# Optimization experiments

Hardware: AMD Instinct MI355X
Metric: run time of the kernel (lower is better)

The kernel has to match this reference:

```python
import jax, jax.numpy as jnp
import numpy as np

B, K, D = 32768, 4096, 256


def setup_inputs() -> dict:
    key = jax.random.key(0)
    k1, k2 = jax.random.split(key)
    z_e_x = jax.random.normal(k1, (B, D), dtype=jnp.float32)
    # embedding.weight initialized N(0, 1) per init='normal'
    weight = jax.random.normal(k2, (K, D), dtype=jnp.float32)
    return {"z_e_x": z_e_x, "weight": weight}


def reference(z_e_x, weight):
    # Squared L2 distances ||z - e||^2 = ||z||^2 - 2 z.e + ||e||^2,
    # computed via a GEMM instead of materializing the [B, K, D] broadcast
    # that the torch code builds with repeat(). Same math as
    # sum((z_e_x_ - codebook_vectors)**2, dim=-1).
    z_sq = jnp.sum(z_e_x * z_e_x, axis=-1, keepdims=True)          # [B, 1]
    e_sq = jnp.sum(weight * weight, axis=-1)                        # [K]
    cross = jnp.einsum('bd,kd->bk', z_e_x, weight)                  # [B, K]
    distances = z_sq - 2.0 * cross + e_sq                           # [B, K]
    # greedy=True path of forward()
    index = jnp.argmin(distances, axis=-1)                          # [B] int
    # straight_through(): quantized lookup + straight-through estimator
    z_q_x = weight[index]                                           # [B, D]
    sg_z_e_x = z_e_x + jax.lax.stop_gradient(z_q_x - z_e_x)         # [B, D]
    return (sg_z_e_x, z_q_x, index)
```

## Files before the change

kernel.cpp:

```cpp
#include <hip/hip_runtime.h>

typedef _Float16 half8 __attribute__((ext_vector_type(8)));
typedef _Float16 half4 __attribute__((ext_vector_type(4)));
typedef float floatx16 __attribute__((ext_vector_type(16)));

constexpr int Bn = 32768, Kn = 4096, Dn = 256;
constexpr int BM = 128;
constexpr int BNS = 64;
constexpr int NI = Kn / BNS;
constexpr int NCH = NI * 4;
constexpr size_t W16_PLANE = (size_t)Kn * Dn * 2;

__global__ void prep_kernel(const float* __restrict__ w, float* __restrict__ esq,
                            _Float16* __restrict__ w16) {
    int code = blockIdx.x * 4 + (threadIdx.x >> 6);
    int lane = threadIdx.x & 63;
    float4 v = *reinterpret_cast<const float4*>(w + (size_t)code * Dn + lane * 4);
    float s = v.x * v.x + v.y * v.y + v.z * v.z + v.w * v.w;
    #pragma unroll
    for (int off = 32; off; off >>= 1) s += __shfl_xor(s, off);
    if (lane == 0) esq[code] = s;
    float fv[4] = {v.x, v.y, v.z, v.w};
    half4 h, l;
    #pragma unroll
    for (int j = 0; j < 4; ++j) {
        _Float16 hh = (_Float16)fv[j];
        h[j] = hh;
        l[j] = (_Float16)(fv[j] - (float)hh);
    }
    _Float16* hi = w16 + (size_t)code * Dn + lane * 4;
    *reinterpret_cast<half4*>(hi) = h;
    *reinterpret_cast<half4*>(hi + (size_t)Kn * Dn) = l;
}

#define GLDS(gsrc, ldsoff)                                                        \
    __builtin_amdgcn_global_load_lds(                                             \
        (const __attribute__((address_space(1))) unsigned int*)(const void*)(gsrc),\
        (__attribute__((address_space(3))) unsigned int*)(void*)(smem + (ldsoff)), \
        16, 0, 0)

__launch_bounds__(512, 2)
__global__ void vq_kernel(const float* __restrict__ z, const float* __restrict__ w,
                          const float* __restrict__ esq, const _Float16* __restrict__ w16,
                          float* __restrict__ out0, float* __restrict__ out1,
                          float* __restrict__ out2) {
    __shared__ char smem[84480];
    const int tid = threadIdx.x;
    const int wv_ = tid >> 6, l = tid & 63;
    const int mw = wv_ >> 1, nw = wv_ & 1;
    const int lh = l >> 5, ll = l & 31;
    const int blkRow = blockIdx.x * BM;

    float* esq_s = reinterpret_cast<float*>(smem + 65536);
    #pragma unroll
    for (int j = 0; j < 8; ++j) esq_s[j * 512 + tid] = esq[j * 512 + tid];

    half8 a_hi[16], a_lo[16];
    {
        const float* zr = z + (size_t)(blkRow + mw * 32 + ll) * Dn + lh * 8;
        #pragma unroll
        for (int ks = 0; ks < 16; ++ks) {
            float4 f0 = *reinterpret_cast<const float4*>(zr + ks * 16);
            float4 f1 = *reinterpret_cast<const float4*>(zr + ks * 16 + 4);
            float fv[8] = {f0.x, f0.y, f0.z, f0.w, f1.x, f1.y, f1.z, f1.w};
            #pragma unroll
            for (int j = 0; j < 8; ++j) {
                _Float16 h = (_Float16)fv[j];
                a_hi[ks][j] = h;
                a_lo[ks][j] = (_Float16)(fv[j] - (float)h);
            }
        }
    }

    const int sc = tid >> 3;
    const int se = ((tid & 7) * 16) ^ ((sc & 7) << 4);
    const char* srcH = reinterpret_cast<const char*>(w16) + (size_t)sc * 512 + se;
    const char* srcL = srcH + W16_PLANE;

    int vks[4];
    {
        const int c_loc = nw * 32 + ll;
        const int swz = (c_loc & 7) << 4;
        #pragma unroll
        for (int ks = 0; ks < 4; ++ks) vks[ks] = c_loc * 128 + ((ks * 32 + lh * 16) ^ swz);
    }

    float rbv[16];
    int rbi[16];
    #pragma unroll
    for (int q = 0; q < 16; ++q) { rbv[q] = 3.4e38f; rbi[q] = 0; }

    __syncthreads();

    GLDS(srcH, 0 + wv_ * 1024);
    GLDS(srcL, 0 + 8192 + wv_ * 1024);
    GLDS(srcH + 128, 16384 + wv_ * 1024);
    GLDS(srcL + 128, 16384 + 8192 + wv_ * 1024);

    for (int ni = 0; ni < NI; ++ni) {
        floatx16 acc = {};
        #pragma unroll
        for (int kc = 0; kc < 4; ++kc) {
            if (ni == NI - 1 && kc == 3) asm volatile("s_waitcnt vmcnt(0)" ::: "memory");
            else                         asm volatile("s_waitcnt vmcnt(2)" ::: "memory");
            __builtin_amdgcn_s_barrier();
            asm volatile("" ::: "memory");
            {
                const int c2 = ni * 4 + kc + 2;
                if (c2 < NCH) {
                    const size_t off2 = (size_t)(c2 >> 2) * 32768 + (size_t)(c2 & 3) * 128;
                    const int b2 = ((kc + 2) & 3) * 16384;
                    GLDS(srcH + off2, b2 + wv_ * 1024);
                    GLDS(srcL + off2, b2 + 8192 + wv_ * 1024);
                }
            }
            __builtin_amdgcn_s_setprio(1);
            #pragma unroll
            for (int ks = 0; ks < 4; ++ks) {
                const half8 bh = *reinterpret_cast<const half8*>(smem + kc * 16384 + vks[ks]);
                const half8 bl = *reinterpret_cast<const half8*>(smem + kc * 16384 + 8192 + vks[ks]);
                const half8 ah = a_hi[kc * 4 + ks];
                const half8 al = a_lo[kc * 4 + ks];
                acc = __builtin_amdgcn_mfma_f32_32x32x16_f16(ah, bh, acc, 0, 0, 0);
                acc = __builtin_amdgcn_mfma_f32_32x32x16_f16(ah, bl, acc, 0, 0, 0);
                acc = __builtin_amdgcn_mfma_f32_32x32x16_f16(al, bh, acc, 0, 0, 0);
            }
            __builtin_amdgcn_s_setprio(0);
        }
        const int col = ni * 64 + nw * 32 + ll;
        const float e = esq_s[col];
        #pragma unroll
        for (int q = 0; q < 16; ++q) {
            float v = fmaf(-2.f, acc[q], e);
            if (v < rbv[q]) { rbv[q] = v; rbi[q] = col; }
        }
    }

    #pragma unroll
    for (int off = 1; off < 32; off <<= 1) {
        #pragma unroll
        for (int q = 0; q < 16; ++q) {
            float ov = __shfl_xor(rbv[q], off);
            int oi = __shfl_xor(rbi[q], off);
            if (ov < rbv[q] || (ov == rbv[q] && oi < rbi[q])) { rbv[q] = ov; rbi[q] = oi; }
        }
    }

    int2* comb = reinterpret_cast<int2*>(smem + 81920);
    if (ll == 0) {
        #pragma unroll
        for (int q = 0; q < 16; ++q) {
            int row = mw * 32 + (q & 3) + 8 * (q >> 2) + 4 * lh;
            comb[row * 2 + nw] = make_int2(__float_as_int(rbv[q]), rbi[q]);
        }
    }
    __syncthreads();
    int* idxF = reinterpret_cast<int*>(smem + 83968);
    if (tid < 128) {
        int2 c0 = comb[tid * 2], c1 = comb[tid * 2 + 1];
        float v0 = __int_as_float(c0.x), v1 = __int_as_float(c1.x);
        idxF[tid] = (v1 < v0 || (v1 == v0 && c1.y < c0.y)) ? c1.y : c0.y;
    }
    __syncthreads();

    {
        const int r = tid >> 2, p4 = tid & 3;
        const int gRow = blkRow + r;
        const int idx = idxF[r];
        const float* wr = w + (size_t)idx * Dn + p4 * 64;
        const float* zr = z + (size_t)gRow * Dn + p4 * 64;
        float* o0 = out0 + (size_t)gRow * Dn + p4 * 64;
        float* o1 = out1 + (size_t)gRow * Dn + p4 * 64;
        #pragma unroll
        for (int q = 0; q < 16; ++q) {
            float4 wq = *reinterpret_cast<const float4*>(wr + q * 4);
            float4 zq = *reinterpret_cast<const float4*>(zr + q * 4);
            *reinterpret_cast<float4*>(o1 + q * 4) = wq;
            float4 sg;
            sg.x = zq.x + (wq.x - zq.x);
            sg.y = zq.y + (wq.y - zq.y);
            sg.z = zq.z + (wq.z - zq.z);
            sg.w = zq.w + (wq.w - zq.w);
            *reinterpret_cast<float4*>(o0 + q * 4) = sg;
        }
        if (p4 == 0) out2[gRow] = (float)idx;
    }
}

extern "C" void kernel_launch(void* const* d_in, const int* in_sizes, int n_in,
                              void* d_out, int out_size, void* d_ws, size_t ws_size,
                              hipStream_t stream) {
    (void)in_sizes; (void)n_in; (void)out_size; (void)ws_size;
    const float* z = (const float*)d_in[0];
    const float* w = (const float*)d_in[1];
    float* esq = (float*)d_ws;
    _Float16* w16 = (_Float16*)((char*)d_ws + 16384);
    float* out0 = (float*)d_out;
    float* out1 = out0 + (size_t)Bn * Dn;
    float* out2 = out1 + (size_t)Bn * Dn;

    prep_kernel<<<Kn / 4, 256, 0, stream>>>(w, esq, w16);
    vq_kernel<<<Bn / BM, 512, 0, stream>>>(z, w, esq, w16, out0, out1, out2);
}
```

Baseline: 291.3 us.

## Give each wave two 32-row M tiles and interleave hi/lo codebook planes

Halves the block to 4 waves, each computing two 32-row tiles so every LDS-loaded B fragment feeds twice as many MFMAs. Prep now writes the codebook hi/lo fp16 halves interleaved per row with a 16-way XOR swizzle, which changes the global-to-LDS load pattern and waits. The aim is fewer LDS reads per MFMA, at the cost of doubled A-fragment and argmin registers, lower occupancy (launch bounds 256,1), and fewer waves to hide latency.

```diff
diff --git a/kernel.cpp b/kernel.cpp
--- a/kernel.cpp
+++ b/kernel.cpp
@@ -9,28 +9,31 @@
 constexpr int BNS = 64;
 constexpr int NI = Kn / BNS;
 constexpr int NCH = NI * 4;
-constexpr size_t W16_PLANE = (size_t)Kn * Dn * 2;
 
 __global__ void prep_kernel(const float* __restrict__ w, float* __restrict__ esq,
-                            _Float16* __restrict__ w16) {
+                            char* __restrict__ w16) {
     int code = blockIdx.x * 4 + (threadIdx.x >> 6);
-    int lane = threadIdx.x & 63;
-    float4 v = *reinterpret_cast<const float4*>(w + (size_t)code * Dn + lane * 4);
+    int l = threadIdx.x & 63;
+    float4 v = *reinterpret_cast<const float4*>(w + (size_t)code * Dn + l * 4);
     float s = v.x * v.x + v.y * v.y + v.z * v.z + v.w * v.w;
     #pragma unroll
     for (int off = 32; off; off >>= 1) s += __shfl_xor(s, off);
-    if (lane == 0) esq[code] = s;
+    if (l == 0) esq[code] = s;
+
     float fv[4] = {v.x, v.y, v.z, v.w};
-    half4 h, l;
+    half4 h, lo;
     #pragma unroll
     for (int j = 0; j < 4; ++j) {
         _Float16 hh = (_Float16)fv[j];
         h[j] = hh;
-        l[j] = (_Float16)(fv[j] - (float)hh);
-    }
-    _Float16* hi = w16 + (size_t)code * Dn + lane * 4;
-    *reinterpret_cast<half4*>(hi) = h;
-    *reinterpret_cast<half4*>(hi + (size_t)Kn * Dn) = l;
+        lo[j] = (_Float16)(fv[j] - (float)hh);
+    }
+    const int kc = l >> 4;
+    const int o_h = (l & 15) * 8;
+    const int swz = (code & 15) << 4;
+    char* row = w16 + (size_t)code * 1024 + kc * 256;
+    *reinterpret_cast<half4*>(row + (o_h ^ swz)) = h;
+    *reinterpret_cast<half4*>(row + ((o_h + 128) ^ swz)) = lo;
 }
 
 #define GLDS(gsrc, ldsoff)                                                        \
@@ -39,25 +42,28 @@
         (__attribute__((address_space(3))) unsigned int*)(void*)(smem + (ldsoff)), \
         16, 0, 0)
 
-__launch_bounds__(512, 2)
+#define MFMA(a, b, c) __builtin_amdgcn_mfma_f32_32x32x16_f16((a), (b), (c), 0, 0, 0)
+
+__launch_bounds__(256, 1)
 __global__ void vq_kernel(const float* __restrict__ z, const float* __restrict__ w,
-                          const float* __restrict__ esq, const _Float16* __restrict__ w16,
+                          const float* __restrict__ esq, const char* __restrict__ w16,
                           float* __restrict__ out0, float* __restrict__ out1,
                           float* __restrict__ out2) {
     __shared__ char smem[84480];
     const int tid = threadIdx.x;
-    const int wv_ = tid >> 6, l = tid & 63;
-    const int mw = wv_ >> 1, nw = wv_ & 1;
+    const int wv = tid >> 6, l = tid & 63;
+    const int mw = wv >> 1, nw = wv & 1;
     const int lh = l >> 5, ll = l & 31;
     const int blkRow = blockIdx.x * BM;
 
     float* esq_s = reinterpret_cast<float*>(smem + 65536);
     #pragma unroll
-    for (int j = 0; j < 8; ++j) esq_s[j * 512 + tid] = esq[j * 512 + tid];
-
-    half8 a_hi[16], a_lo[16];
-    {
-        const float* zr = z + (size_t)(blkRow + mw * 32 + ll) * Dn + lh * 8;
+    for (int j = 0; j < 16; ++j) esq_s[j * 256 + tid] = esq[j * 256 + tid];
+
+    half8 a_hi[2][16], a_lo[2][16];
+    #pragma unroll
+    for (int t = 0; t < 2; ++t) {
+        const float* zr = z + (size_t)(blkRow + mw * 64 + t * 32 + ll) * Dn + lh * 8;
         #pragma unroll
         for (int ks = 0; ks < 16; ++ks) {
             float4 f0 = *reinterpret_cast<const float4*>(zr + ks * 16);
@@ -66,73 +72,85 @@
             #pragma unroll
             for (int j = 0; j < 8; ++j) {
                 _Float16 h = (_Float16)fv[j];
-                a_hi[ks][j] = h;
-                a_lo[ks][j] = (_Float16)(fv[j] - (float)h);
+                a_hi[t][ks][j] = h;
+                a_lo[t][ks][j] = (_Float16)(fv[j] - (float)h);
             }
         }
     }
 
-    const int sc = tid >> 3;
-    const int se = ((tid & 7) * 16) ^ ((sc & 7) << 4);
-    const char* srcH = reinterpret_cast<const char*>(w16) + (size_t)sc * 512 + se;
-    const char* srcL = srcH + W16_PLANE;
-
-    int vks[4];
+    const int G0 = wv * 256 + l;
+    const size_t srcOff0 = (size_t)(G0 >> 4) * 1024 + (G0 & 15) * 16;
+
+    int addrH[4], addrL[4];
     {
         const int c_loc = nw * 32 + ll;
-        const int swz = (c_loc & 7) << 4;
-        #pragma unroll
-        for (int ks = 0; ks < 4; ++ks) vks[ks] = c_loc * 128 + ((ks * 32 + lh * 16) ^ swz);
-    }
-
-    float rbv[16];
-    int rbi[16];
-    #pragma unroll
-    for (int q = 0; q < 16; ++q) { rbv[q] = 3.4e38f; rbi[q] = 0; }
-
-    __syncthreads();
-
-    GLDS(srcH, 0 + wv_ * 1024);
-    GLDS(srcL, 0 + 8192 + wv_ * 1024);
-    GLDS(srcH + 128, 16384 + wv_ * 1024);
-    GLDS(srcL + 128, 16384 + 8192 + wv_ * 1024);
+        const int swz = (c_loc & 15) << 4;
+        #pragma unroll
+        for (int ks = 0; ks < 4; ++ks) {
+            const int o = ks * 32 + lh * 16;
+            addrH[ks] = c_loc * 256 + (o ^ swz);
+            addrL[ks] = c_loc * 256 + ((o + 128) ^ swz);
+        }
+    }
+
+    float rbv0[16], rbv1[16];
+    int rbi0[16], rbi1[16];
+    #pragma unroll
+    for (int q = 0; q < 16; ++q) { rbv0[q] = 3.4e38f; rbv1[q] = 3.4e38f; rbi0[q] = 0; rbi1[q] = 0; }
+
+    asm volatile("s_waitcnt vmcnt(0)" ::: "memory");
+    __syncthreads();
+
+    {
+        const char* s0 = w16 + srcOff0;
+        const char* s1 = w16 + 256 + srcOff0;
+        const int d0 = wv * 4096, d1 = 16384 + wv * 4096;
+        GLDS(s0, d0); GLDS(s0 + 4096, d0 + 1024); GLDS(s0 + 8192, d0 + 2048); GLDS(s0 + 12288, d0 + 3072);
+        GLDS(s1, d1); GLDS(s1 + 4096, d1 + 1024); GLDS(s1 + 8192, d1 + 2048); GLDS(s1 + 12288, d1 + 3072);
+    }
 
     for (int ni = 0; ni < NI; ++ni) {
-        floatx16 acc = {};
+        floatx16 acc0 = {}, acc1 = {};
         #pragma unroll
         for (int kc = 0; kc < 4; ++kc) {
-            if (ni == NI - 1 && kc == 3) asm volatile("s_waitcnt vmcnt(0)" ::: "memory");
-            else                         asm volatile("s_waitcnt vmcnt(2)" ::: "memory");
+            const int c = ni * 4 + kc;
+            if (c + 2 < NCH) {
+                const char* s2 = w16 + (size_t)((c + 2) >> 2) * 65536 + ((c + 2) & 3) * 256 + srcOff0;
+                const int d2 = (((kc + 2) & 3) * 16384) + wv * 4096;
+                GLDS(s2, d2); GLDS(s2 + 4096, d2 + 1024);
+                GLDS(s2 + 8192, d2 + 2048); GLDS(s2 + 12288, d2 + 3072);
+                asm volatile("s_waitcnt vmcnt(8)" ::: "memory");
+            } else if (c + 1 < NCH) {
+                asm volatile("s_waitcnt vmcnt(4)" ::: "memory");
+            } else {
+                asm volatile("s_waitcnt vmcnt(0)" ::: "memory");
+            }
             __builtin_amdgcn_s_barrier();
             asm volatile("" ::: "memory");
-            {
-                const int c2 = ni * 4 + kc + 2;
-                if (c2 < NCH) {
-                    const size_t off2 = (size_t)(c2 >> 2) * 32768 + (size_t)(c2 & 3) * 128;
-                    const int b2 = ((kc + 2) & 3) * 16384;
-                    GLDS(srcH + off2, b2 + wv_ * 1024);
-                    GLDS(srcL + off2, b2 + 8192 + wv_ * 1024);
-                }
-            }
+            const char* base = smem + kc * 16384;
             __builtin_amdgcn_s_setprio(1);
             #pragma unroll
             for (int ks = 0; ks < 4; ++ks) {
-                const half8 bh = *reinterpret_cast<const half8*>(smem + kc * 16384 + vks[ks]);
-                const half8 bl = *reinterpret_cast<const half8*>(smem + kc * 16384 + 8192 + vks[ks]);
-                const half8 ah = a_hi[kc * 4 + ks];
-                const half8 al = a_lo[kc * 4 + ks];
-                acc = __builtin_amdgcn_mfma_f32_32x32x16_f16(ah, bh, acc, 0, 0, 0);
-                acc = __builtin_amdgcn_mfma_f32_32x32x16_f16(ah, bl, acc, 0, 0, 0);
-                acc = __builtin_amdgcn_mfma_f32_32x32x16_f16(al, bh, acc, 0, 0, 0);
+                const half8 bh = *reinterpret_cast<const half8*>(base + addrH[ks]);
+                const half8 bl = *reinterpret_cast<const half8*>(base + addrL[ks]);
+                const int ksg = kc * 4 + ks;
+                acc0 = MFMA(a_hi[0][ksg], bh, acc0);
+                acc1 = MFMA(a_hi[1][ksg], bh, acc1);
+                acc0 = MFMA(a_hi[0][ksg], bl, acc0);
+                acc1 = MFMA(a_hi[1][ksg], bl, acc1);
+                acc0 = MFMA(a_lo[0][ksg], bh, acc0);
+                acc1 = MFMA(a_lo[1][ksg], bh, acc1);
             }
             __builtin_amdgcn_s_setprio(0);
         }
+        const float e = esq_s[ni * 64 + nw * 32 + ll];
         const int col = ni * 64 + nw * 32 + ll;
-        const float e = esq_s[col];
         #pragma unroll
         for (int q = 0; q < 16; ++q) {
-            float v = fmaf(-2.f, acc[q], e);
-            if (v < rbv[q]) { rbv[q] = v; rbi[q] = col; }
+            const float v0 = fmaf(-2.f, acc0[q], e);
+            if (v0 < rbv0[q]) { rbv0[q] = v0; rbi0[q] = col; }
+            const float v1 = fmaf(-2.f, acc1[q], e);
+            if (v1 < rbv1[q]) { rbv1[q] = v1; rbi1[q] = col; }
         }
     }
 
@@ -140,18 +158,21 @@
     for (int off = 1; off < 32; off <<= 1) {
         #pragma unroll
         for (int q = 0; q < 16; ++q) {
-            float ov = __shfl_xor(rbv[q], off);
-            int oi = __shfl_xor(rbi[q], off);
-            if (ov < rbv[q] || (ov == rbv[q] && oi < rbi[q])) { rbv[q] = ov; rbi[q] = oi; }
-        }
-    }
-
+            float ov0 = __shfl_xor(rbv0[q], off); int oi0 = __shfl_xor(rbi0[q], off);
+            if (ov0 < rbv0[q] || (ov0 == rbv0[q] && oi0 < rbi0[q])) { rbv0[q] = ov0; rbi0[q] = oi0; }
+            float ov1 = __shfl_xor(rbv1[q], off); int oi1 = __shfl_xor(rbi1[q], off);
+            if (ov1 < rbv1[q] || (ov1 == rbv1[q] && oi1 < rbi1[q])) { rbv1[q] = ov1; rbi1[q] = oi1; }
+        }
+    }
+
+    __syncthreads();
     int2* comb = reinterpret_cast<int2*>(smem + 81920);
     if (ll == 0) {
         #pragma unroll
         for (int q = 0; q < 16; ++q) {
-            int row = mw * 32 + (q & 3) + 8 * (q >> 2) + 4 * lh;
-            comb[row * 2 + nw] = make_int2(__float_as_int(rbv[q]), rbi[q]);
+            const int r32 = (q & 3) + 8 * (q >> 2) + 4 * lh;
+            comb[(mw * 64 + r32) * 2 + nw] = make_int2(__float_as_int(rbv0[q]), rbi0[q]);
+            comb[(mw * 64 + 32 + r32) * 2 + nw] = make_int2(__float_as_int(rbv1[q]), rbi1[q]);
         }
     }
     __syncthreads();
@@ -164,15 +185,15 @@
     __syncthreads();
 
     {
-        const int r = tid >> 2, p4 = tid & 3;
+        const int r = tid >> 1, p2 = tid & 1;
         const int gRow = blkRow + r;
         const int idx = idxF[r];
-        const float* wr = w + (size_t)idx * Dn + p4 * 64;
-        const float* zr = z + (size_t)gRow * Dn + p4 * 64;
-        float* o0 = out0 + (size_t)gRow * Dn + p4 * 64;
-        float* o1 = out1 + (size_t)gRow * Dn + p4 * 64;
-        #pragma unroll
-        for (int q = 0; q < 16; ++q) {
+        const float* wr = w + (size_t)idx * Dn + p2 * 128;
+        const float* zr = z + (size_t)gRow * Dn + p2 * 128;
+        float* o0 = out0 + (size_t)gRow * Dn + p2 * 128;
+        float* o1 = out1 + (size_t)gRow * Dn + p2 * 128;
+        #pragma unroll
+        for (int q = 0; q < 32; ++q) {
             float4 wq = *reinterpret_cast<const float4*>(wr + q * 4);
             float4 zq = *reinterpret_cast<const float4*>(zr + q * 4);
             *reinterpret_cast<float4*>(o1 + q * 4) = wq;
@@ -183,7 +204,7 @@
             sg.w = zq.w + (wq.w - zq.w);
             *reinterpret_cast<float4*>(o0 + q * 4) = sg;
         }
-        if (p4 == 0) out2[gRow] = (float)idx;
+        if (p2 == 0) out2[gRow] = (float)idx;
     }
 }
 
@@ -194,11 +215,11 @@
     const float* z = (const float*)d_in[0];
     const float* w = (const float*)d_in[1];
     float* esq = (float*)d_ws;
-    _Float16* w16 = (_Float16*)((char*)d_ws + 16384);
+    char* w16 = (char*)d_ws + 16384;
     float* out0 = (float*)d_out;
     float* out1 = out0 + (size_t)Bn * Dn;
     float* out2 = out1 + (size_t)Bn * Dn;
 
     prep_kernel<<<Kn / 4, 256, 0, stream>>>(w, esq, w16);
-    vq_kernel<<<Bn / BM, 512, 0, stream>>>(z, w, esq, w16, out0, out1, out2);
+    vq_kernel<<<Bn / BM, 256, 0, stream>>>(z, w, esq, w16, out0, out1, out2);
 }
```

Result: slower. 319.0 us (+9.5%).
